# Kernel optimization log

Hardware: AMD Instinct MI355X
Metric: run time of the kernel (lower is better)

Reference implementation:

```python
import jax, jax.numpy as jnp
import numpy as np

K = 4
EPS = 1e-5
NEG_SLOPE = 0.2


def _edge_feature(coor_q, x_q, coor_k, x_k, k):
    """coor_*: [B,3,G*], x_q: [B,C,Gq], x_k: [B,C,Gk] -> [B,2C,Gq,k]"""
    B = x_k.shape[0]
    cq = jax.lax.stop_gradient(coor_q)
    ck = jax.lax.stop_gradient(coor_k)
    # squared pairwise distances [B, Gq, Gk]
    q2 = jnp.sum(cq * cq, axis=1)  # [B,Gq]
    k2 = jnp.sum(ck * ck, axis=1)  # [B,Gk]
    dist = q2[:, :, None] + k2[:, None, :] - 2.0 * jnp.einsum('bcq,bck->bqk', cq, ck)
    _, idx = jax.lax.top_k(-dist, k)  # k nearest, idx: [B,Gq,k]
    xk_t = jnp.transpose(x_k, (0, 2, 1))  # [B,Gk,C]
    feat = xk_t[jnp.arange(B)[:, None, None], idx]  # [B,Gq,k,C] gather
    feat = jnp.transpose(feat, (0, 3, 1, 2))  # [B,C,Gq,k]
    xq = jnp.broadcast_to(x_q[:, :, :, None], feat.shape)
    return jnp.concatenate([feat - xq, xq], axis=1)


def _group_norm(x, gamma, beta, groups):
    # x: [B,C,G,k], normalize per (group, sample) over (C//groups, G, k)
    B, C, G, k = x.shape
    xr = x.reshape(B, groups, -1)
    mean = jnp.mean(xr, axis=-1, keepdims=True)
    var = jnp.var(xr, axis=-1, keepdims=True)
    xn = ((xr - mean) * jax.lax.rsqrt(var + EPS)).reshape(B, C, G, k)
    return xn * gamma[None, :, None, None] + beta[None, :, None, None]


def _block(x, W, gamma, beta):
    # 1x1 conv (no bias) + GroupNorm(4) + LeakyReLU(0.2)
    y = jnp.einsum('oc,bcgk->bogk', W, x)
    y = _group_norm(y, gamma, beta, 4)
    return jax.nn.leaky_relu(y, NEG_SLOPE)


def setup_inputs() -> dict:
    key = jax.random.key(0)
    ks = jax.random.split(key, 10)
    B, C, Gs, Gd = 16, 384, 4096, 1024
    return {
        'coor': jax.random.normal(ks[0], (B, 3, Gs), jnp.float32),
        'f': jax.random.normal(ks[1], (B, C, Gs), jnp.float32),
        'coor_q': jax.random.normal(ks[2], (B, 3, Gd), jnp.float32),
        'f_q': jax.random.normal(ks[3], (B, C, Gd), jnp.float32),
        'W1': jax.random.normal(ks[4], (512, 2 * C), jnp.float32) * 0.02,
        'g1': jnp.ones((512,), jnp.float32),
        'b1': jnp.zeros((512,), jnp.float32),
        'W2': jax.random.normal(ks[5], (C, 1024), jnp.float32) * 0.02,
        'g2': jnp.ones((C,), jnp.float32),
        'b2': jnp.zeros((C,), jnp.float32),
    }


def reference(coor, f, coor_q, f_q, W1, g1, b1, W2, g2, b2):
    e1 = _edge_feature(coor_q, f_q, coor, f, K)        # [B,768,Gd,k]
    h = jnp.max(_block(e1, W1, g1, b1), axis=-1)       # [B,512,Gd]
    e2 = _edge_feature(coor_q, h, coor_q, h, K)        # [B,1024,Gd,k]
    out = jnp.max(_block(e2, W2, g2, b2), axis=-1)     # [B,384,Gd]
    return out
```

## Files before the change

### kernel.cpp

```cpp
#include <hip/hip_runtime.h>
#include <stdint.h>

#define B_   16
#define CIN  384
#define GS   4096
#define GD   1024
#define M1   512
#define K2C  512
#define M2   384
#define ROWS2 768
#define NEG  0.2f
#define EPS_ 1e-5f

typedef __bf16 bf16x8 __attribute__((ext_vector_type(8)));
typedef float  f32x4  __attribute__((ext_vector_type(4)));
typedef float  f32x2  __attribute__((ext_vector_type(2)));
typedef unsigned long long u64k;

__device__ __forceinline__ float bf2f(ushort u) {
  uint32_t v = ((uint32_t)u) << 16;
  return __builtin_bit_cast(float, v);
}
__device__ __forceinline__ ushort f2bf(float f) {
  uint32_t x = __builtin_bit_cast(uint32_t, f);
  x += 0x7FFFu + ((x >> 16) & 1u);
  return (ushort)(x >> 16);
}

__device__ __forceinline__ f32x2 pk_mul(f32x2 a, f32x2 b) {
  f32x2 d; asm("v_pk_mul_f32 %0, %1, %2" : "=v"(d) : "v"(a), "v"(b)); return d;
}
__device__ __forceinline__ f32x2 pk_add(f32x2 a, f32x2 b) {
  f32x2 d; asm("v_pk_add_f32 %0, %1, %2" : "=v"(d) : "v"(a), "v"(b)); return d;
}
__device__ __forceinline__ f32x2 pk_fma(f32x2 a, f32x2 b, f32x2 c) {
  f32x2 d; asm("v_pk_fma_f32 %0, %1, %2, %3" : "=v"(d) : "v"(a), "v"(b), "v"(c)); return d;
}

__global__ void k_transpose(const float* __restrict__ src, ushort* __restrict__ dst,
                            int Cdim, int N) {
  __shared__ ushort tile[32][33];
  int b = blockIdx.z;
  int n0 = blockIdx.x * 32, c0 = blockIdx.y * 32;
  const float* s = src + (size_t)b * Cdim * N;
  ushort* d = dst + (size_t)b * Cdim * N;
  int tx = threadIdx.x, ty = threadIdx.y;
#pragma unroll
  for (int i = 0; i < 4; i++) {
    int c = c0 + ty + i * 8;
    tile[ty + i * 8][tx] = f2bf(s[(size_t)c * N + n0 + tx]);
  }
  __syncthreads();
#pragma unroll
  for (int i = 0; i < 4; i++) {
    int n = n0 + ty + i * 8;
    d[(size_t)n * Cdim + c0 + tx] = tile[tx][ty + i * 8];
  }
}

__global__ void k_wprep2(const float* __restrict__ W1, const float* __restrict__ W2,
                         ushort* __restrict__ W1a, ushort* __restrict__ W1d,
                         ushort* __restrict__ W2a, ushort* __restrict__ W2d) {
  int blk = blockIdx.x;
  if (blk < 768) {
    int t = blk * 256 + threadIdx.x;
    int o = t / 384, c = t % 384;
    float wa = W1[(size_t)o * 768 + c];
    float wb = W1[(size_t)o * 768 + 384 + c];
    W1a[t] = f2bf(wa);
    W1d[t] = f2bf(wb - wa);
  } else {
    int t = (blk - 768) * 256 + threadIdx.x;
    int o = t / 512, c = t % 512;
    float wa = W2[(size_t)o * 1024 + c];
    float wb = W2[(size_t)o * 1024 + 512 + c];
    W2a[t] = f2bf(wa);
    W2d[t] = f2bf(wb - wa);
  }
}

__global__ void k_s2both(const float* __restrict__ cs, const float* __restrict__ cq,
                         float* __restrict__ s2s, float* __restrict__ s2q) {
#pragma clang fp contract(off)
  int b = blockIdx.z;
  int i = blockIdx.x * 256 + threadIdx.x;
  if (i < GS) {
    const float* cb = cs + (size_t)b * 3 * GS;
    float x = cb[i], y = cb[GS + i], z = cb[2 * GS + i];
    s2s[(size_t)b * GS + i] = (x * x + y * y) + z * z;
  } else {
    int j = i - GS;
    const float* cb = cq + (size_t)b * 3 * GD;
    float x = cb[j], y = cb[GD + j], z = cb[2 * GD + j];
    s2q[(size_t)b * GD + j] = (x * x + y * y) + z * z;
  }
}

__device__ __forceinline__ uint32_t dmap(float d) {
  uint32_t u = __builtin_bit_cast(uint32_t, d);
  return u ^ (((uint32_t)((int32_t)u >> 31)) | 0x80000000u);
}
__device__ __forceinline__ void kce(u64k& a, u64k& b) {
  bool c = b < a;
  u64k lo = c ? b : a, hi = c ? a : b;
  a = lo; b = hi;
}
__device__ __forceinline__ void klmin(u64k& a, u64k b) { a = b < a ? b : a; }

template<int GSRC>
__global__ __launch_bounds__(256) void k_knn(const float* __restrict__ cq,
                                             const float* __restrict__ ck,
                                             const float* __restrict__ s2qry,
                                             const float* __restrict__ s2src,
                                             int* __restrict__ idx) {
  constexpr int ITERS = GSRC / 256;
  static_assert(ITERS % 2 == 0, "even iteration count required for 2-deep unroll");
  int tid = threadIdx.x;
  int lane = tid & 63, wv = tid >> 6;
  int b = blockIdx.y;
  int q = blockIdx.x * 4 + wv;
  const float* cqb = cq + (size_t)b * 3 * GD;
  const float* ckb = ck + (size_t)b * 3 * GSRC;
  const float* s2b = s2src + (size_t)b * GSRC;
  float qx = cqb[q], qy = cqb[GD + q], qz = cqb[2 * GD + q];
  float q2 = s2qry[(size_t)b * GD + q];
  f32x2 qxp = {qx, qx}, qyp = {qy, qy}, qzp = {qz, qz};
  f32x2 q2p = {q2, q2}, m2p = {-2.f, -2.f};

  u64k k0 = ~0ull, k1 = ~0ull, k2 = ~0ull, k3 = ~0ull;
  uint32_t thr = 0xFFFFFFFFu;

#define KNN_STEP(Xv, Yv, Zv, Sv, J0)                                           \
  {                                                                            \
    f32x2 xl = {Xv.x, Xv.y}, xh = {Xv.z, Xv.w};                                \
    f32x2 yl = {Yv.x, Yv.y}, yh = {Yv.z, Yv.w};                                \
    f32x2 zl = {Zv.x, Zv.y}, zh = {Zv.z, Zv.w};                                \
    f32x2 sl = {Sv.x, Sv.y}, sh = {Sv.z, Sv.w};                                \
    f32x2 dotl = pk_add(pk_add(pk_mul(qxp, xl), pk_mul(qyp, yl)), pk_mul(qzp, zl)); \
    f32x2 doth = pk_add(pk_add(pk_mul(qxp, xh), pk_mul(qyp, yh)), pk_mul(qzp, zh)); \
    f32x2 dl = pk_fma(dotl, m2p, pk_add(q2p, sl));                             \
    f32x2 dh = pk_fma(doth, m2p, pk_add(q2p, sh));                             \
    uint32_t u0 = dmap(dl.x), u1 = dmap(dl.y), u2 = dmap(dh.x), u3 = dmap(dh.y); \
    uint32_t umin = min(min(u0, u1), min(u2, u3));                             \
    if (__any(umin < thr)) {                                                   \
      u64k n0 = ((u64k)u0 << 32) | (uint32_t)(J0);                             \
      u64k n1 = ((u64k)u1 << 32) | (uint32_t)((J0) + 1);                       \
      u64k n2 = ((u64k)u2 << 32) | (uint32_t)((J0) + 2);                       \
      u64k n3 = ((u64k)u3 << 32) | (uint32_t)((J0) + 3);                       \
      kce(n0, n1); kce(n2, n3); kce(n0, n2); kce(n1, n3); kce(n1, n2);         \
      klmin(k0, n3); klmin(k1, n2); klmin(k2, n1); klmin(k3, n0);              \
      kce(k0, k2); kce(k1, k3); kce(k0, k1); kce(k2, k3);                      \
      thr = (uint32_t)(k3 >> 32);                                              \
    }                                                                          \
  }

#define KNN_LOAD(Xv, Yv, Zv, Sv, J)                                            \
  {                                                                            \
    Xv = *reinterpret_cast<const float4*>(ckb + (J));                          \
    Yv = *reinterpret_cast<const float4*>(ckb + GSRC + (J));                   \
    Zv = *reinterpret_cast<const float4*>(ckb + 2 * GSRC + (J));               \
    Sv = *reinterpret_cast<const float4*>(s2b + (J));                          \
  }

  int base = lane * 4;
  float4 X0, Y0, Z0, S0, X1, Y1, Z1, S1;
  KNN_LOAD(X0, Y0, Z0, S0, base);
  for (int it = 0; it < ITERS; it += 2) {
    int j0 = it * 256 + base;
    KNN_LOAD(X1, Y1, Z1, S1, j0 + 256);
    KNN_STEP(X0, Y0, Z0, S0, j0);
    if (it + 2 < ITERS) KNN_LOAD(X0, Y0, Z0, S0, j0 + 512);
    KNN_STEP(X1, Y1, Z1, S1, j0 + 256);
  }
#undef KNN_STEP
#undef KNN_LOAD

#pragma unroll
  for (int off = 1; off < 64; off <<= 1) {
    u64k p0 = __shfl_xor(k0, off), p1 = __shfl_xor(k1, off);
    u64k p2 = __shfl_xor(k2, off), p3 = __shfl_xor(k3, off);
    klmin(k0, p3); klmin(k1, p2); klmin(k2, p1); klmin(k3, p0);
    kce(k0, k2); kce(k1, k3); kce(k0, k1); kce(k2, k3);
  }
  if (lane == 0) {
    int4 r;
    r.x = (int)(uint32_t)k0; r.y = (int)(uint32_t)k1;
    r.z = (int)(uint32_t)k2; r.w = (int)(uint32_t)k3;
    *reinterpret_cast<int4*>(&idx[((size_t)b * GD + q) * 4]) = r;
  }
}

template<bool OUT_BF16>
__global__ __launch_bounds__(256) void k_gemm(const ushort* __restrict__ W,
                                              const ushort* __restrict__ Xt,
                                              void* __restrict__ outv,
                                              int M, int Kd, int N) {
  __shared__ __align__(16) ushort As[128 * 40];
  __shared__ __align__(16) ushort Bs[128 * 40];
  int b = blockIdx.z;
  const ushort* X = Xt + (size_t)b * N * Kd;
  int m0 = blockIdx.y * 128, n0 = blockIdx.x * 128;
  int tid = threadIdx.x;
  int w = tid >> 6, lane = tid & 63;
  int lr = lane & 15, lq = lane >> 4;
  int mw = (w >> 1) * 64, nw = (w & 1) * 64;
  int r0 = tid >> 2, c0 = tid & 3;

  f32x4 zero = {0.f, 0.f, 0.f, 0.f};
  f32x4 acc[4][4];
#pragma unroll
  for (int mi = 0; mi < 4; mi++)
#pragma unroll
    for (int ni = 0; ni < 4; ni++) acc[mi][ni] = zero;

  int nk = Kd / 32;
  for (int kt = 0; kt < nk; kt++) {
    int kk = kt * 32;
    __syncthreads();
    uint4 va0 = *reinterpret_cast<const uint4*>(W + (size_t)(m0 + r0) * Kd + kk + c0 * 8);
    uint4 va1 = *reinterpret_cast<const uint4*>(W + (size_t)(m0 + r0 + 64) * Kd + kk + c0 * 8);
    uint4 vb0 = *reinterpret_cast<const uint4*>(X + (size_t)(n0 + r0) * Kd + kk + c0 * 8);
    uint4 vb1 = *reinterpret_cast<const uint4*>(X + (size_t)(n0 + r0 + 64) * Kd + kk + c0 * 8);
    *reinterpret_cast<uint4*>(&As[(r0)      * 40 + c0 * 8]) = va0;
    *reinterpret_cast<uint4*>(&As[(r0 + 64) * 40 + c0 * 8]) = va1;
    *reinterpret_cast<uint4*>(&Bs[(r0)      * 40 + c0 * 8]) = vb0;
    *reinterpret_cast<uint4*>(&Bs[(r0 + 64) * 40 + c0 * 8]) = vb1;
    __syncthreads();
    bf16x8 af[4], bfr[4];
#pragma unroll
    for (int mi = 0; mi < 4; mi++)
      af[mi] = *reinterpret_cast<const bf16x8*>(&As[(mw + mi * 16 + lr) * 40 + lq * 8]);
#pragma unroll
    for (int ni = 0; ni < 4; ni++)
      bfr[ni] = *reinterpret_cast<const bf16x8*>(&Bs[(nw + ni * 16 + lr) * 40 + lq * 8]);
#pragma unroll
    for (int mi = 0; mi < 4; mi++)
#pragma unroll
      for (int ni = 0; ni < 4; ni++)
        acc[mi][ni] = __builtin_amdgcn_mfma_f32_16x16x32_bf16(af[mi], bfr[ni], acc[mi][ni], 0, 0, 0);
  }
#pragma unroll
  for (int mi = 0; mi < 4; mi++) {
    int m = m0 + mw + mi * 16 + lq * 4;
#pragma unroll
    for (int ni = 0; ni < 4; ni++) {
      int n = n0 + nw + ni * 16 + lr;
#pragma unroll
      for (int r = 0; r < 4; r++) {
        size_t off = (size_t)b * M * N + (size_t)(m + r) * N + n;
        if constexpr (OUT_BF16) ((ushort*)outv)[off] = f2bf(acc[mi][ni][r]);
        else                    ((float*)outv)[off] = acc[mi][ni][r];
      }
    }
  }
}

__global__ __launch_bounds__(256) void k_stats1y(const ushort* __restrict__ A,
                                                 const float* __restrict__ Bq,
                                                 const int* __restrict__ idx1,
                                                 const float* __restrict__ gam,
                                                 float* __restrict__ Ysel,
                                                 float* __restrict__ part) {
  __shared__ __align__(16) ushort Arow[GS];
  __shared__ __align__(16) int ids[GD * 4];
  __shared__ float rs[256], rq[256];
  int s = blockIdx.x, grp = blockIdx.y, b = blockIdx.z;
  int tid = threadIdx.x;
  for (int i = tid; i < GD; i += 256) {
    int4 v = *reinterpret_cast<const int4*>(&idx1[((size_t)b * GD + i) * 4]);
    v.x &= (GS - 1); v.y &= (GS - 1); v.z &= (GS - 1); v.w &= (GS - 1);
    *reinterpret_cast<int4*>(&ids[i * 4]) = v;
  }
  float sum = 0.f, ssq = 0.f;
  for (int oi = 0; oi < 16; oi++) {
    int o = grp * 128 + s * 16 + oi;
    const ushort* Ar = A + ((size_t)b * M1 + o) * GS;
    __syncthreads();
#pragma unroll
    for (int i = tid * 8; i < GS; i += 2048)
      *reinterpret_cast<uint4*>(&Arow[i]) = *reinterpret_cast<const uint4*>(&Ar[i]);
    __syncthreads();
    const float* Br = Bq + ((size_t)b * M1 + o) * GD;
    float* Yr = Ysel + ((size_t)b * M1 + o) * GD;
    float sgn = gam[o];
    for (int g = tid; g < GD; g += 256) {
      int4 id = *reinterpret_cast<const int4*>(&ids[g * 4]);
      float base = Br[g];
      float y0 = bf2f(Arow[id.x]) + base;
      float y1 = bf2f(Arow[id.y]) + base;
      float y2 = bf2f(Arow[id.z]) + base;
      float y3 = bf2f(Arow[id.w]) + base;
      sum += y0 + y1 + y2 + y3;
      ssq += y0 * y0 + y1 * y1 + y2 * y2 + y3 * y3;
      float mx = fmaxf(fmaxf(y0, y1), fmaxf(y2, y3));
      float mn = fminf(fminf(y0, y1), fminf(y2, y3));
      Yr[g] = (sgn >= 0.f) ? mx : mn;
    }
  }
  rs[tid] = sum; rq[tid] = ssq;
  __syncthreads();
  for (int t = 128; t > 0; t >>= 1) {
    if (tid < t) { rs[tid] += rs[tid + t]; rq[tid] += rq[tid + t]; }
    __syncthreads();
  }
  if (tid == 0) {
    int key = ((b * 4 + grp) * 8 + s) * 2;
    part[key] = rs[0]; part[key + 1] = rq[0];
  }
}

__global__ __launch_bounds__(256) void k_stats2y(const float* __restrict__ Y2,
                                                 const int* __restrict__ idx2,
                                                 const float* __restrict__ gam,
                                                 float* __restrict__ Ysel,
                                                 float* __restrict__ part) {
  __shared__ __align__(16) float Arow[GD];
  __shared__ __align__(16) int ids[GD * 4];
  __shared__ float rs[256], rq[256];
  int s = blockIdx.x, grp = blockIdx.y, b = blockIdx.z;
  int tid = threadIdx.x;
  for (int i = tid; i < GD; i += 256) {
    int4 v = *reinterpret_cast<const int4*>(&idx2[((size_t)b * GD + i) * 4]);
    v.x &= (GD - 1); v.y &= (GD - 1); v.z &= (GD - 1); v.w &= (GD - 1);
    *reinterpret_cast<int4*>(&ids[i * 4]) = v;
  }
  float sum = 0.f, ssq = 0.f;
  for (int oi = 0; oi < 12; oi++) {
    int o = grp * 96 + s * 12 + oi;
    const float* Ar = Y2 + ((size_t)b * ROWS2 + o) * GD;
    __syncthreads();
#pragma unroll
    for (int i = tid * 4; i < GD; i += 1024)
      *reinterpret_cast<float4*>(&Arow[i]) = *reinterpret_cast<const float4*>(&Ar[i]);
    __syncthreads();
    const float* Br = Y2 + ((size_t)b * ROWS2 + 384 + o) * GD;
    float* Yr = Ysel + ((size_t)b * M2 + o) * GD;
    float sgn = gam[o];
    for (int g = tid; g < GD; g += 256) {
      int4 id = *reinterpret_cast<const int4*>(&ids[g * 4]);
      float base = Br[g];
      float y0 = Arow[id.x] + base;
      float y1 = Arow[id.y] + base;
      float y2 = Arow[id.z] + base;
      float y3 = Arow[id.w] + base;
      sum += y0 + y1 + y2 + y3;
      ssq += y0 * y0 + y1 * y1 + y2 * y2 + y3 * y3;
      float mx = fmaxf(fmaxf(y0, y1), fmaxf(y2, y3));
      float mn = fminf(fminf(y0, y1), fminf(y2, y3));
      Yr[g] = (sgn >= 0.f) ? mx : mn;
    }
  }
  rs[tid] = sum; rq[tid] = ssq;
  __syncthreads();
  for (int t = 128; t > 0; t >>= 1) {
    if (tid < t) { rs[tid] += rs[tid + t]; rq[tid] += rq[tid + t]; }
    __syncthreads();
  }
  if (tid == 0) {
    int key = ((b * 4 + grp) * 8 + s) * 2;
    part[key] = rs[0]; part[key + 1] = rq[0];
  }
}

__global__ void k_statsfin(const float* __restrict__ part, float* __restrict__ fin, float invN) {
  int t = threadIdx.x;
  float s = 0.f, q = 0.f;
  for (int i = 0; i < 8; i++) { s += part[(t * 8 + i) * 2]; q += part[(t * 8 + i) * 2 + 1]; }
  float mean = s * invN;
  float var = q * invN - mean * mean;
  float rstd = 1.0f / sqrtf(fmaxf(var, 0.0f) + EPS_);
  fin[t * 2] = mean; fin[t * 2 + 1] = rstd;
}

__global__ void k_h2(const float* __restrict__ Ysel, const float* __restrict__ fin,
                     const float* __restrict__ gam, const float* __restrict__ bet,
                     ushort* __restrict__ hT) {
  __shared__ ushort tile[64][66];
  int g0 = blockIdx.x * 64, o0 = blockIdx.y * 64, b = blockIdx.z;
  int tid = threadIdx.x;
  int gx = tid & 63, oy = tid >> 6;
#pragma unroll
  for (int oi = 0; oi < 16; oi++) {
    int ol = oi * 4 + oy;
    int o = o0 + ol;
    float y = Ysel[((size_t)b * M1 + o) * GD + g0 + gx];
    float mean = fin[(b * 4 + (o >> 7)) * 2];
    float rstd = fin[(b * 4 + (o >> 7)) * 2 + 1];
    float v = (y - mean) * rstd * gam[o] + bet[o];
    v = v >= 0.f ? v : NEG * v;
    tile[ol][gx] = f2bf(v);
  }
  __syncthreads();
  int col = tid & 63, r4 = tid >> 6;
#pragma unroll
  for (int i = 0; i < 16; i++) {
    int gl = i * 4 + r4;
    hT[((size_t)b * GD + g0 + gl) * K2C + o0 + col] = tile[col][gl];
  }
}

__global__ void k_out2(const float* __restrict__ Ysel2, const float* __restrict__ fin,
                       const float* __restrict__ gam, const float* __restrict__ bet,
                       float* __restrict__ out) {
  int b = blockIdx.z, o = blockIdx.y;
  int g = blockIdx.x * 256 + threadIdx.x;
  float mean = fin[(b * 4 + o / 96) * 2];
  float rstd = fin[(b * 4 + o / 96) * 2 + 1];
  float y = Ysel2[((size_t)b * M2 + o) * GD + g];
  float v = (y - mean) * rstd * gam[o] + bet[o];
  v = v >= 0.f ? v : NEG * v;
  out[((size_t)b * M2 + o) * GD + g] = v;
}

extern "C" void kernel_launch(void* const* d_in, const int* in_sizes, int n_in,
                              void* d_out, int out_size, void* d_ws, size_t ws_size,
                              hipStream_t stream) {
  (void)in_sizes; (void)n_in; (void)out_size;
  const float* coor  = (const float*)d_in[0];
  const float* f     = (const float*)d_in[1];
  const float* coorq = (const float*)d_in[2];
  const float* fq    = (const float*)d_in[3];
  const float* W1    = (const float*)d_in[4];
  const float* g1    = (const float*)d_in[5];
  const float* b1    = (const float*)d_in[6];
  const float* W2    = (const float*)d_in[7];
  const float* g2    = (const float*)d_in[8];
  const float* b2    = (const float*)d_in[9];

  if (ws_size < 182468608u) return;

  char* ws = (char*)d_ws;
  int*    idx1 = (int*)(ws + 0);
  int*    idx2 = (int*)(ws + 0x40000);
  float*  s1p  = (float*)(ws + 0x80000);
  float*  s1f  = (float*)(ws + 0x81000);
  float*  s2p  = (float*)(ws + 0x82000);
  float*  s2f  = (float*)(ws + 0x83000);
  ushort* W1a  = (ushort*)(ws + 0x84000);
  ushort* W1d  = W1a + (size_t)512 * 384;
  ushort* W2a  = W1d + (size_t)512 * 384;
  ushort* W2d  = W2a + (size_t)384 * 512;
  ushort* fT   = W2d + (size_t)384 * 512;
  ushort* fqT  = fT + (size_t)B_ * GS * CIN;
  ushort* Abuf = fqT + (size_t)B_ * GD * CIN;
  float*  Bq   = (float*)(Abuf + (size_t)B_ * M1 * GS);
  ushort* hT   = (ushort*)((char*)Bq + (size_t)B_ * M1 * GD * 4);
  float*  Y2   = (float*)fT;
  float*  Ysel1 = (float*)fT;
  float*  Ysel2 = (float*)Abuf;
  float*  s2s  = (float*)hT;
  float*  s2q  = s2s + (size_t)B_ * GS;

  k_transpose<<<dim3(GS / 32, CIN / 32, B_), dim3(32, 8), 0, stream>>>(f, fT, CIN, GS);
  k_transpose<<<dim3(GD / 32, CIN / 32, B_), dim3(32, 8), 0, stream>>>(fq, fqT, CIN, GD);
  k_wprep2<<<dim3(1536), 256, 0, stream>>>(W1, W2, W1a, W1d, W2a, W2d);
  k_s2both<<<dim3((GS + GD) / 256, 1, B_), 256, 0, stream>>>(coor, coorq, s2s, s2q);

  k_knn<GS><<<dim3(GD / 4, B_), 256, 0, stream>>>(coorq, coor, s2q, s2s, idx1);
  k_knn<GD><<<dim3(GD / 4, B_), 256, 0, stream>>>(coorq, coorq, s2q, s2q, idx2);

  k_gemm<true ><<<dim3(GS / 128, M1 / 128, B_), 256, 0, stream>>>(W1a, fT, Abuf, M1, CIN, GS);
  k_gemm<false><<<dim3(GD / 128, M1 / 128, B_), 256, 0, stream>>>(W1d, fqT, Bq, M1, CIN, GD);

  k_stats1y<<<dim3(8, 4, B_), 256, 0, stream>>>(Abuf, Bq, idx1, g1, Ysel1, s1p);
  k_statsfin<<<1, 64, 0, stream>>>(s1p, s1f, 1.0f / 524288.0f);
  k_h2<<<dim3(GD / 64, M1 / 64, B_), 256, 0, stream>>>(Ysel1, s1f, g1, b1, hT);

  k_gemm<false><<<dim3(GD / 128, ROWS2 / 128, B_), 256, 0, stream>>>(W2a, hT, Y2, ROWS2, K2C, GD);

  k_stats2y<<<dim3(8, 4, B_), 256, 0, stream>>>(Y2, idx2, g2, Ysel2, s2p);
  k_statsfin<<<1, 64, 0, stream>>>(s2p, s2f, 1.0f / 393216.0f);
  k_out2<<<dim3(GD / 256, M2, B_), 256, 0, stream>>>(Ysel2, s2f, g2, b2, (float*)d_out);
}
```

Before: 457.9 us.

## Process two queries per wavefront in kNN and fold stats finalize into consumers

The kNN kernel now has each wavefront handle two query points, so every loaded source-point tile is reused for both queries and half as many blocks are launched. The warp-vote early-exit threshold test is removed, so the sorting network now runs unconditionally for every candidate batch. The separate statsfin kernels are dropped, and k_h2 and k_out2 recompute mean and rstd from the partial sums themselves, saving two tiny launches at the cost of redundant per-block reductions. Key packing uses a bitcast helper instead of shift-or.

Measured after the change: 451.0 us. Within noise of the previous version (-1.5%).

```diff
diff --git a/kernel.cpp b/kernel.cpp
--- a/kernel.cpp
+++ b/kernel.cpp
@@ -100,6 +100,10 @@
   uint32_t u = __builtin_bit_cast(uint32_t, d);
   return u ^ (((uint32_t)((int32_t)u >> 31)) | 0x80000000u);
 }
+__device__ __forceinline__ u64k mkkey(uint32_t hi, uint32_t lo) {
+  uint2 t; t.x = lo; t.y = hi;
+  return __builtin_bit_cast(u64k, t);
+}
 __device__ __forceinline__ void kce(u64k& a, u64k& b) {
   bool c = b < a;
   u64k lo = c ? b : a, hi = c ? a : b;
@@ -118,17 +122,36 @@
   int tid = threadIdx.x;
   int lane = tid & 63, wv = tid >> 6;
   int b = blockIdx.y;
-  int q = blockIdx.x * 4 + wv;
+  int qA = blockIdx.x * 8 + wv * 2;
+  int qB = qA + 1;
   const float* cqb = cq + (size_t)b * 3 * GD;
   const float* ckb = ck + (size_t)b * 3 * GSRC;
   const float* s2b = s2src + (size_t)b * GSRC;
-  float qx = cqb[q], qy = cqb[GD + q], qz = cqb[2 * GD + q];
-  float q2 = s2qry[(size_t)b * GD + q];
-  f32x2 qxp = {qx, qx}, qyp = {qy, qy}, qzp = {qz, qz};
-  f32x2 q2p = {q2, q2}, m2p = {-2.f, -2.f};
-
-  u64k k0 = ~0ull, k1 = ~0ull, k2 = ~0ull, k3 = ~0ull;
-  uint32_t thr = 0xFFFFFFFFu;
+  float qxA = cqb[qA], qyA = cqb[GD + qA], qzA = cqb[2 * GD + qA];
+  float qxB = cqb[qB], qyB = cqb[GD + qB], qzB = cqb[2 * GD + qB];
+  float q2A = s2qry[(size_t)b * GD + qA];
+  float q2B = s2qry[(size_t)b * GD + qB];
+  f32x2 qxpA = {qxA, qxA}, qypA = {qyA, qyA}, qzpA = {qzA, qzA}, q2pA = {q2A, q2A};
+  f32x2 qxpB = {qxB, qxB}, qypB = {qyB, qyB}, qzpB = {qzB, qzB}, q2pB = {q2B, q2B};
+  f32x2 m2p = {-2.f, -2.f};
+
+  u64k kA0 = ~0ull, kA1 = ~0ull, kA2 = ~0ull, kA3 = ~0ull;
+  u64k kB0 = ~0ull, kB1 = ~0ull, kB2 = ~0ull, kB3 = ~0ull;
+
+#define KNN_Q(QXP, QYP, QZP, Q2P, K0, K1, K2, K3)                              \
+  {                                                                            \
+    f32x2 dotl = pk_add(pk_add(pk_mul(QXP, xl), pk_mul(QYP, yl)), pk_mul(QZP, zl)); \
+    f32x2 doth = pk_add(pk_add(pk_mul(QXP, xh), pk_mul(QYP, yh)), pk_mul(QZP, zh)); \
+    f32x2 dl = pk_fma(dotl, m2p, pk_add(Q2P, sl));                             \
+    f32x2 dh = pk_fma(doth, m2p, pk_add(Q2P, sh));                             \
+    u64k n0 = mkkey(dmap(dl.x), j0u);                                          \
+    u64k n1 = mkkey(dmap(dl.y), j0u + 1);                                      \
+    u64k n2 = mkkey(dmap(dh.x), j0u + 2);                                      \
+    u64k n3 = mkkey(dmap(dh.y), j0u + 3);                                      \
+    kce(n0, n1); kce(n2, n3); kce(n0, n2); kce(n1, n3); kce(n1, n2);           \
+    klmin(K0, n3); klmin(K1, n2); klmin(K2, n1); klmin(K3, n0);                \
+    kce(K0, K2); kce(K1, K3); kce(K0, K1); kce(K2, K3);                        \
+  }
 
 #define KNN_STEP(Xv, Yv, Zv, Sv, J0)                                           \
   {                                                                            \
@@ -136,22 +159,9 @@
     f32x2 yl = {Yv.x, Yv.y}, yh = {Yv.z, Yv.w};                                \
     f32x2 zl = {Zv.x, Zv.y}, zh = {Zv.z, Zv.w};                                \
     f32x2 sl = {Sv.x, Sv.y}, sh = {Sv.z, Sv.w};                                \
-    f32x2 dotl = pk_add(pk_add(pk_mul(qxp, xl), pk_mul(qyp, yl)), pk_mul(qzp, zl)); \
-    f32x2 doth = pk_add(pk_add(pk_mul(qxp, xh), pk_mul(qyp, yh)), pk_mul(qzp, zh)); \
-    f32x2 dl = pk_fma(dotl, m2p, pk_add(q2p, sl));                             \
-    f32x2 dh = pk_fma(doth, m2p, pk_add(q2p, sh));                             \
-    uint32_t u0 = dmap(dl.x), u1 = dmap(dl.y), u2 = dmap(dh.x), u3 = dmap(dh.y); \
-    uint32_t umin = min(min(u0, u1), min(u2, u3));                             \
-    if (__any(umin < thr)) {                                                   \
-      u64k n0 = ((u64k)u0 << 32) | (uint32_t)(J0);                             \
-      u64k n1 = ((u64k)u1 << 32) | (uint32_t)((J0) + 1);                       \
-      u64k n2 = ((u64k)u2 << 32) | (uint32_t)((J0) + 2);                       \
-      u64k n3 = ((u64k)u3 << 32) | (uint32_t)((J0) + 3);                       \
-      kce(n0, n1); kce(n2, n3); kce(n0, n2); kce(n1, n3); kce(n1, n2);         \
-      klmin(k0, n3); klmin(k1, n2); klmin(k2, n1); klmin(k3, n0);              \
-      kce(k0, k2); kce(k1, k3); kce(k0, k1); kce(k2, k3);                      \
-      thr = (uint32_t)(k3 >> 32);                                              \
-    }                                                                          \
+    uint32_t j0u = (uint32_t)(J0);                                             \
+    KNN_Q(qxpA, qypA, qzpA, q2pA, kA0, kA1, kA2, kA3);                         \
+    KNN_Q(qxpB, qypB, qzpB, q2pB, kB0, kB1, kB2, kB3);                         \
   }
 
 #define KNN_LOAD(Xv, Yv, Zv, Sv, J)                                            \
@@ -173,20 +183,29 @@
     KNN_STEP(X1, Y1, Z1, S1, j0 + 256);
   }
 #undef KNN_STEP
+#undef KNN_Q
 #undef KNN_LOAD
 
 #pragma unroll
   for (int off = 1; off < 64; off <<= 1) {
-    u64k p0 = __shfl_xor(k0, off), p1 = __shfl_xor(k1, off);
-    u64k p2 = __shfl_xor(k2, off), p3 = __shfl_xor(k3, off);
-    klmin(k0, p3); klmin(k1, p2); klmin(k2, p1); klmin(k3, p0);
-    kce(k0, k2); kce(k1, k3); kce(k0, k1); kce(k2, k3);
+    u64k p0 = __shfl_xor(kA0, off), p1 = __shfl_xor(kA1, off);
+    u64k p2 = __shfl_xor(kA2, off), p3 = __shfl_xor(kA3, off);
+    klmin(kA0, p3); klmin(kA1, p2); klmin(kA2, p1); klmin(kA3, p0);
+    kce(kA0, kA2); kce(kA1, kA3); kce(kA0, kA1); kce(kA2, kA3);
+    u64k r0 = __shfl_xor(kB0, off), r1 = __shfl_xor(kB1, off);
+    u64k r2 = __shfl_xor(kB2, off), r3 = __shfl_xor(kB3, off);
+    klmin(kB0, r3); klmin(kB1, r2); klmin(kB2, r1); klmin(kB3, r0);
+    kce(kB0, kB2); kce(kB1, kB3); kce(kB0, kB1); kce(kB2, kB3);
   }
   if (lane == 0) {
-    int4 r;
-    r.x = (int)(uint32_t)k0; r.y = (int)(uint32_t)k1;
-    r.z = (int)(uint32_t)k2; r.w = (int)(uint32_t)k3;
-    *reinterpret_cast<int4*>(&idx[((size_t)b * GD + q) * 4]) = r;
+    int4 ra;
+    ra.x = (int)(uint32_t)kA0; ra.y = (int)(uint32_t)kA1;
+    ra.z = (int)(uint32_t)kA2; ra.w = (int)(uint32_t)kA3;
+    *reinterpret_cast<int4*>(&idx[((size_t)b * GD + qA) * 4]) = ra;
+    int4 rb;
+    rb.x = (int)(uint32_t)kB0; rb.y = (int)(uint32_t)kB1;
+    rb.z = (int)(uint32_t)kB2; rb.w = (int)(uint32_t)kB3;
+    *reinterpret_cast<int4*>(&idx[((size_t)b * GD + qB) * 4]) = rb;
   }
 }
 
@@ -362,30 +381,25 @@
   }
 }
 
-__global__ void k_statsfin(const float* __restrict__ part, float* __restrict__ fin, float invN) {
-  int t = threadIdx.x;
-  float s = 0.f, q = 0.f;
-  for (int i = 0; i < 8; i++) { s += part[(t * 8 + i) * 2]; q += part[(t * 8 + i) * 2 + 1]; }
-  float mean = s * invN;
-  float var = q * invN - mean * mean;
-  float rstd = 1.0f / sqrtf(fmaxf(var, 0.0f) + EPS_);
-  fin[t * 2] = mean; fin[t * 2 + 1] = rstd;
-}
-
-__global__ void k_h2(const float* __restrict__ Ysel, const float* __restrict__ fin,
+__global__ void k_h2(const float* __restrict__ Ysel, const float* __restrict__ part,
                      const float* __restrict__ gam, const float* __restrict__ bet,
                      ushort* __restrict__ hT) {
   __shared__ ushort tile[64][66];
   int g0 = blockIdx.x * 64, o0 = blockIdx.y * 64, b = blockIdx.z;
   int tid = threadIdx.x;
+  int tkey = b * 4 + (o0 >> 7);
+  float s = 0.f, q = 0.f;
+#pragma unroll
+  for (int i = 0; i < 8; i++) { s += part[(tkey * 8 + i) * 2]; q += part[(tkey * 8 + i) * 2 + 1]; }
+  float mean = s * (1.0f / 524288.0f);
+  float var = q * (1.0f / 524288.0f) - mean * mean;
+  float rstd = 1.0f / sqrtf(fmaxf(var, 0.0f) + EPS_);
   int gx = tid & 63, oy = tid >> 6;
 #pragma unroll
   for (int oi = 0; oi < 16; oi++) {
     int ol = oi * 4 + oy;
     int o = o0 + ol;
     float y = Ysel[((size_t)b * M1 + o) * GD + g0 + gx];
-    float mean = fin[(b * 4 + (o >> 7)) * 2];
-    float rstd = fin[(b * 4 + (o >> 7)) * 2 + 1];
     float v = (y - mean) * rstd * gam[o] + bet[o];
     v = v >= 0.f ? v : NEG * v;
     tile[ol][gx] = f2bf(v);
@@ -399,13 +413,18 @@
   }
 }
 
-__global__ void k_out2(const float* __restrict__ Ysel2, const float* __restrict__ fin,
+__global__ void k_out2(const float* __restrict__ Ysel2, const float* __restrict__ part,
                        const float* __restrict__ gam, const float* __restrict__ bet,
                        float* __restrict__ out) {
   int b = blockIdx.z, o = blockIdx.y;
   int g = blockIdx.x * 256 + threadIdx.x;
-  float mean = fin[(b * 4 + o / 96) * 2];
-  float rstd = fin[(b * 4 + o / 96) * 2 + 1];
+  int tkey = b * 4 + o / 96;
+  float s = 0.f, q = 0.f;
+#pragma unroll
+  for (int i = 0; i < 8; i++) { s += part[(tkey * 8 + i) * 2]; q += part[(tkey * 8 + i) * 2 + 1]; }
+  float mean = s * (1.0f / 393216.0f);
+  float var = q * (1.0f / 393216.0f) - mean * mean;
+  float rstd = 1.0f / sqrtf(fmaxf(var, 0.0f) + EPS_);
   float y = Ysel2[((size_t)b * M2 + o) * GD + g];
   float v = (y - mean) * rstd * gam[o] + bet[o];
   v = v >= 0.f ? v : NEG * v;
@@ -433,9 +452,7 @@
   int*    idx1 = (int*)(ws + 0);
   int*    idx2 = (int*)(ws + 0x40000);
   float*  s1p  = (float*)(ws + 0x80000);
-  float*  s1f  = (float*)(ws + 0x81000);
   float*  s2p  = (float*)(ws + 0x82000);
-  float*  s2f  = (float*)(ws + 0x83000);
   ushort* W1a  = (ushort*)(ws + 0x84000);
   ushort* W1d  = W1a + (size_t)512 * 384;
   ushort* W2a  = W1d + (size_t)512 * 384;
@@ -456,19 +473,17 @@
   k_wprep2<<<dim3(1536), 256, 0, stream>>>(W1, W2, W1a, W1d, W2a, W2d);
   k_s2both<<<dim3((GS + GD) / 256, 1, B_), 256, 0, stream>>>(coor, coorq, s2s, s2q);
 
-  k_knn<GS><<<dim3(GD / 4, B_), 256, 0, stream>>>(coorq, coor, s2q, s2s, idx1);
-  k_knn<GD><<<dim3(GD / 4, B_), 256, 0, stream>>>(coorq, coorq, s2q, s2q, idx2);
+  k_knn<GS><<<dim3(GD / 8, B_), 256, 0, stream>>>(coorq, coor, s2q, s2s, idx1);
+  k_knn<GD><<<dim3(GD / 8, B_), 256, 0, stream>>>(coorq, coorq, s2q, s2q, idx2);
 
   k_gemm<true ><<<dim3(GS / 128, M1 / 128, B_), 256, 0, stream>>>(W1a, fT, Abuf, M1, CIN, GS);
   k_gemm<false><<<dim3(GD / 128, M1 / 128, B_), 256, 0, stream>>>(W1d, fqT, Bq, M1, CIN, GD);
 
   k_stats1y<<<dim3(8, 4, B_), 256, 0, stream>>>(Abuf, Bq, idx1, g1, Ysel1, s1p);
-  k_statsfin<<<1, 64, 0, stream>>>(s1p, s1f, 1.0f / 524288.0f);
-  k_h2<<<dim3(GD / 64, M1 / 64, B_), 256, 0, stream>>>(Ysel1, s1f, g1, b1, hT);
+  k_h2<<<dim3(GD / 64, M1 / 64, B_), 256, 0, stream>>>(Ysel1, s1p, g1, b1, hT);
 
   k_gemm<false><<<dim3(GD / 128, ROWS2 / 128, B_), 256, 0, stream>>>(W2a, hT, Y2, ROWS2, K2C, GD);
 
   k_stats2y<<<dim3(8, 4, B_), 256, 0, stream>>>(Y2, idx2, g2, Ysel2, s2p);
-  k_statsfin<<<1, 64, 0, stream>>>(s2p, s2f, 1.0f / 393216.0f);
-  k_out2<<<dim3(GD / 256, M2, B_), 256, 0, stream>>>(Ysel2, s2f, g2, b2, (float*)d_out);
-}
+  k_out2<<<dim3(GD / 256, M2, B_), 256, 0, stream>>>(Ysel2, s2p, g2, b2, (float*)d_out);
+}
```
